# Optimization experiments

Hardware: AMD Instinct MI355X
Metric: run time of the kernel (lower is better)

The kernel has to match this reference:

```python
import jax, jax.numpy as jnp
import numpy as np

B, S, D, A = 8, 4096, 128, 128


def _pos_encoding(seq_len, dim):
    # sin/cos positional encoding, same construction as the torch buffer
    pos = np.arange(seq_len, dtype=np.float32)[:, None]
    div = np.exp(np.arange(0, dim, 2, dtype=np.float32) * (-np.log(10000.0) / dim))
    pe = np.zeros((seq_len, dim), dtype=np.float32)
    pe[:, 0::2] = np.sin(pos * div)
    pe[:, 1::2] = np.cos(pos * div)
    return jnp.asarray(pe)


def setup_inputs() -> dict:
    key = jax.random.key(0)
    ks = jax.random.split(key, 7)
    sc = 1.0 / np.sqrt(D)
    return {
        "x": jax.random.normal(ks[0], (B, S, D), dtype=jnp.float32),
        "Wq": jax.random.normal(ks[1], (D, A), dtype=jnp.float32) * sc,
        "bq": jnp.zeros((A,), dtype=jnp.float32),
        "Wk": jax.random.normal(ks[2], (D, A), dtype=jnp.float32) * sc,
        "bk": jnp.zeros((A,), dtype=jnp.float32),
        "Wv": jax.random.normal(ks[3], (D, A), dtype=jnp.float32) * sc,
        "bv": jnp.zeros((A,), dtype=jnp.float32),
    }


def reference(x, Wq, bq, Wk, bk, Wv, bv):
    b, s, d = x.shape
    pe = _pos_encoding(s, d)  # [S, D]
    xp = x + pe[None]  # broadcast add of positional encoding
    q = xp @ Wq + bq  # [B, S, A]
    k = xp @ Wk + bk
    v = xp @ Wv + bv
    scale = 1.0 / jnp.sqrt(jnp.asarray(Wq.shape[1], dtype=jnp.float32))
    scores = jnp.einsum("bsa,bta->bst", q, k) * scale  # [B, S, S]
    weights = jax.nn.softmax(scores, axis=-1)
    out = jnp.einsum("bst,bta->bsa", weights, v)  # [B, S, A]
    return out
```

## Files before the change

### kernel.cpp

```cpp
#include <hip/hip_runtime.h>

#define BB 8
#define SS 4096
#define DD 128

typedef __attribute__((ext_vector_type(8))) short v8s;
typedef __attribute__((ext_vector_type(4))) short v4s;
typedef __attribute__((ext_vector_type(4))) float v4f;
typedef __attribute__((ext_vector_type(16))) float v16f;

__device__ __forceinline__ unsigned short f2bf(float f) {
    unsigned int u = __float_as_uint(f);
    u += 0x7fffu + ((u >> 16) & 1u);
    return (unsigned short)(u >> 16);
}
__device__ __forceinline__ float bf2f(unsigned short s) {
    return __uint_as_float(((unsigned int)s) << 16);
}
__device__ __forceinline__ unsigned int pk_bf16(float a, float b) {
    unsigned int ua = __float_as_uint(a) + 0x8000u;
    unsigned int ub = __float_as_uint(b) + 0x8000u;
    return __builtin_amdgcn_perm(ub, ua, 0x07060302u);
}

#if !defined(__HIP_DEVICE_COMPILE__)
#define MFMA16(a, b, c) (c)
#define MFMA32(a, b, c) (c)
#else
#define MFMA16(a, b, c) __builtin_amdgcn_mfma_f32_16x16x32_bf16((a), (b), (c), 0, 0, 0)
#define MFMA32(a, b, c) __builtin_amdgcn_mfma_f32_32x32x16_bf16((a), (b), (c), 0, 0, 0)
#endif

#if !defined(__HIP_DEVICE_COMPILE__)
#define EXP2F(x) exp2f(x)
#elif __has_builtin(__builtin_amdgcn_exp2f)
#define EXP2F(x) __builtin_amdgcn_exp2f(x)
#else
#define EXP2F(x) exp2f(x)
#endif

#define QSCALE 0.12751743f
#define FIXM 24.0f

__global__ __launch_bounds__(256) void prep_w_kernel(
    const float* __restrict__ Wq, const float* __restrict__ Wk,
    const float* __restrict__ Wv, unsigned short* __restrict__ Wt)
{
    int id = blockIdx.x * 256 + threadIdx.x;
    int w = id >> 14;
    int n = (id >> 7) & 127;
    int k = id & 127;
    const float* W = (w == 0) ? Wq : (w == 1) ? Wk : Wv;
    Wt[id] = f2bf(W[k * 128 + n]);
}

__global__ __launch_bounds__(256, 3) void proj_kernel(
    const float* __restrict__ x, const unsigned short* __restrict__ Wt,
    const float* __restrict__ bq, const float* __restrict__ bk,
    const float* __restrict__ bv,
    unsigned short* __restrict__ qo, unsigned short* __restrict__ ko,
    unsigned short* __restrict__ vo)
{
    __shared__ __attribute__((aligned(16))) unsigned short o_q[64 * 136];
    __shared__ __attribute__((aligned(16))) unsigned short o_k[64 * 136];
    __shared__ __attribute__((aligned(16))) unsigned short o_v[128 * 72];

    const int tid = threadIdx.x;
    const int wave = tid >> 6;
    const int lane = tid & 63;
    const int quad = lane >> 4;
    const int l15 = lane & 15;
    const int rbase = blockIdx.x * 64;

    const int flatrow = rbase + wave * 16 + l15;
    const int srow = flatrow & 4095;
    v8s af[4];
#pragma unroll
    for (int kc = 0; kc < 4; ++kc) {
        const int kbase = kc * 32 + quad * 8;
        const v4f* xp = (const v4f*)(x + (size_t)flatrow * DD + kbase);
        v4f x0 = xp[0], x1 = xp[1];
        float xv[8] = {x0[0], x0[1], x0[2], x0[3], x1[0], x1[1], x1[2], x1[3]};
        v8s a;
#pragma unroll
        for (int j = 0; j < 8; ++j) {
            int d = kbase + j;
            float freq = __expf((float)(d & ~1) * -0.07195578415606394f);
            float arg = (float)srow * freq;
            float pe = (d & 1) ? __cosf(arg) : __sinf(arg);
            a[j] = (short)f2bf(xv[j] + pe);
        }
        af[kc] = a;
    }

#pragma unroll
    for (int mat = 0; mat < 3; ++mat) {
        const unsigned short* Wp = Wt + (mat << 14);
        const float* bias = (mat == 0) ? bq : (mat == 1) ? bk : bv;
#pragma unroll
        for (int nb = 0; nb < 8; ++nb) {
            const int col = nb * 16 + l15;
            v4f acc = {0.f, 0.f, 0.f, 0.f};
#pragma unroll
            for (int kc = 0; kc < 4; ++kc) {
                v8s bf = *(const v8s*)(Wp + col * 128 + kc * 32 + quad * 8);
                acc = MFMA16(af[kc], bf, acc);
            }
            float bval = bias[col];
#pragma unroll
            for (int reg = 0; reg < 4; ++reg) {
                int lr = wave * 16 + quad * 4 + reg;
                float val = acc[reg] + bval;
                if (mat == 0) {
                    o_q[lr * 136 + col] = f2bf(val * QSCALE);
                } else if (mat == 1) {
                    o_k[lr * 136 + col] = f2bf(val);
                } else {
                    o_v[col * 72 + lr] = f2bf(val);
                }
            }
        }
    }
    __syncthreads();

#pragma unroll
    for (int it = 0; it < 4; ++it) {
        int id = it * 256 + tid;
        int r = id >> 4, c8 = id & 15;
        *(v8s*)(qo + (size_t)(rbase + r) * DD + c8 * 8) =
            *(const v8s*)(o_q + r * 136 + c8 * 8);
        *(v8s*)(ko + (size_t)(rbase + r) * DD + c8 * 8) =
            *(const v8s*)(o_k + r * 136 + c8 * 8);
    }
    const int b0 = rbase >> 12, s0 = rbase & 4095;
#pragma unroll
    for (int it = 0; it < 4; ++it) {
        int id = it * 256 + tid;
        int a = id >> 3, c = id & 7;
        *(v8s*)(vo + ((size_t)(b0 * 128 + a)) * SS + s0 + c * 8) =
            *(const v8s*)(o_v + a * 72 + c * 8);
    }
}

#define KT 32
#define HKEYS 2048
#define NT (HKEYS / KT)
__global__ __launch_bounds__(256, 2) void flash_kernel(
    const unsigned short* __restrict__ qg,
    const unsigned short* __restrict__ kg,
    const unsigned short* __restrict__ vg,
    float* __restrict__ out,
    unsigned short* __restrict__ o2,
    float* __restrict__ statl)
{
    __shared__ __attribute__((aligned(16))) unsigned short k_lds[2][KT * 128];
    __shared__ __attribute__((aligned(16))) unsigned short v_lds[2][128 * KT];

    const int tid = threadIdx.x;
    const int wave = tid >> 6;
    const int lane = tid & 63;
    const int hi = lane >> 5;
    const int l31 = lane & 31;
    const int bid = blockIdx.x;
    const int b = bid & 7;
    const int half = (bid >> 3) & 1;
    const int qt = bid >> 4;
    const int qbase = qt * 128 + wave * 32;

    const size_t qrow = (size_t)(b * SS + qbase + l31) * DD;
    v8s qf[8];
#pragma unroll
    for (int kc = 0; kc < 8; ++kc)
        qf[kc] = *(const v8s*)(qg + qrow + kc * 16 + hi * 8);

    v16f o[4];
#pragma unroll
    for (int fg = 0; fg < 4; ++fg)
#pragma unroll
        for (int r = 0; r < 16; ++r) o[fg][r] = 0.f;
    float lrow = 0.f;

    const unsigned short* kb = kg + (size_t)b * SS * DD + (size_t)half * HKEYS * DD;
    const unsigned short* vb = vg + (size_t)b * DD * SS + half * HKEYS;

    const int kr_r = tid >> 4, kr_c = tid & 15;
    const int va = tid >> 2, vc8 = tid & 3;
    v8s kr[2], vr[2];

    auto load_tile = [&](int t) {
        const unsigned short* kp = kb + (size_t)t * KT * DD;
        const unsigned short* vp = vb + t * KT;
#pragma unroll
        for (int it = 0; it < 2; ++it) {
            kr[it] = *(const v8s*)(kp + (size_t)(kr_r + it * 16) * DD + kr_c * 8);
            vr[it] = *(const v8s*)(vp + (size_t)(va + it * 64) * SS + vc8 * 8);
        }
    };
    auto store_tile = [&](int p) {
#pragma unroll
        for (int it = 0; it < 2; ++it) {
            int r = kr_r + it * 16;
            *(v8s*)(&k_lds[p][r * 128 + ((kr_c ^ (r & 7)) << 3)]) = kr[it];
            int a = va + it * 64;
            v4s lo = {vr[it][0], vr[it][1], vr[it][2], vr[it][3]};
            v4s hv = {vr[it][4], vr[it][5], vr[it][6], vr[it][7]};
            int cc = vc8 >> 1, h = vc8 & 1;
            *(v4s*)(&v_lds[p][a * 32 + (((cc ^ (a & 3)) << 3) + h * 4)]) = lo;
            *(v4s*)(&v_lds[p][a * 32 + ((((cc + 2) ^ (a & 3)) << 3) + h * 4)]) = hv;
        }
    };
    auto compute = [&](int p) {
        v16f s;
#pragma unroll
        for (int r = 0; r < 16; ++r) s[r] = -FIXM;
#pragma unroll
        for (int kc = 0; kc < 8; ++kc) {
            v8s af = *(const v8s*)(&k_lds[p][l31 * 128 +
                                   (((kc * 2 + hi) ^ (l31 & 7)) << 3)]);
            s = MFMA32(af, qf[kc], s);
        }
        float e[16];
#pragma unroll
        for (int r = 0; r < 16; ++r) {
            e[r] = EXP2F(s[r]);
            lrow += e[r];
        }
        union { v8s v[2]; unsigned int u[8]; } P;
#pragma unroll
        for (int g = 0; g < 2; ++g)
#pragma unroll
            for (int m = 0; m < 4; ++m)
                P.u[g * 4 + m] = pk_bf16(e[2 * m + 8 * g], e[2 * m + 8 * g + 1]);
#pragma unroll
        for (int fg = 0; fg < 4; ++fg) {
            int row = fg * 32 + l31;
#pragma unroll
            for (int g = 0; g < 2; ++g) {
                v8s bf = *(const v8s*)(&v_lds[p][row * 32 +
                                       (((2 * hi + g) ^ (row & 3)) << 3)]);
                o[fg] = MFMA32(P.v[g], bf, o[fg]);
            }
        }
    };

    load_tile(0);
    store_tile(0);
    load_tile(1);
    __syncthreads();
#pragma unroll 1
    for (int kt = 0; kt < NT; kt += 2) {
        store_tile(1);
        if (kt + 2 < NT) load_tile(kt + 2);
        compute(0);
        __syncthreads();
        if (kt + 2 < NT) {
            store_tile(0);
            if (kt + 3 < NT) load_tile(kt + 3);
        }
        compute(1);
        __syncthreads();
    }

    lrow += __shfl_xor(lrow, 32, 64);
    if (lane < 32)
        statl[half * (BB * SS) + b * SS + qbase + l31] = lrow;
#pragma unroll
    for (int fg = 0; fg < 4; ++fg)
#pragma unroll
        for (int r = 0; r < 16; ++r) {
            int qr = (r & 3) + 8 * (r >> 2) + 4 * hi;
            size_t idx = (size_t)(b * SS + qbase + qr) * DD + fg * 32 + l31;
            if (half == 0) out[idx] = o[fg][r];
            else           o2[idx] = f2bf(o[fg][r]);
        }
}

__global__ __launch_bounds__(256) void combine_kernel(
    float* __restrict__ out, const unsigned short* __restrict__ o2,
    const float* __restrict__ statl)
{
    int id = blockIdx.x * 256 + threadIdx.x;
    int row = id >> 5;
    int c = (id & 31) * 4;
    float l1 = statl[row], l2 = statl[BB * SS + row];
    float inv = 1.0f / (l1 + l2);
    size_t base = (size_t)row * DD + c;
    v4f o1 = *(v4f*)(out + base);
    v4s p2 = *(const v4s*)(o2 + base);
    v4f r;
#pragma unroll
    for (int j = 0; j < 4; ++j)
        r[j] = (o1[j] + bf2f((unsigned short)p2[j])) * inv;
    *(v4f*)(out + base) = r;
}

extern "C" void kernel_launch(void* const* d_in, const int* in_sizes, int n_in,
                              void* d_out, int out_size, void* d_ws, size_t ws_size,
                              hipStream_t stream)
{
    const float* x  = (const float*)d_in[0];
    const float* Wq = (const float*)d_in[1];
    const float* bq = (const float*)d_in[2];
    const float* Wk = (const float*)d_in[3];
    const float* bk = (const float*)d_in[4];
    const float* Wv = (const float*)d_in[5];
    const float* bv = (const float*)d_in[6];
    float* out = (float*)d_out;

    unsigned short* Wt = (unsigned short*)d_ws;
    unsigned short* q  = Wt + 49152;
    unsigned short* k  = q + (size_t)BB * SS * DD;
    unsigned short* vT = k + (size_t)BB * SS * DD;
    unsigned short* O2 = vT + (size_t)BB * SS * DD;
    float* statl = (float*)(O2 + (size_t)BB * SS * DD);

    hipLaunchKernelGGL(prep_w_kernel, dim3(192), dim3(256), 0, stream, Wq, Wk, Wv, Wt);
    hipLaunchKernelGGL(proj_kernel, dim3(BB * SS / 64), dim3(256), 0, stream,
                       x, Wt, bq, bk, bv, q, k, vT);
    hipLaunchKernelGGL(flash_kernel, dim3(SS / 128 * 2 * BB), dim3(256), 0, stream,
                       q, k, vT, out, O2, statl);
    hipLaunchKernelGGL(combine_kernel, dim3(BB * SS * DD / 4 / 256), dim3(256), 0, stream,
                       out, O2, statl);
}
```

Before: 187.9 us.

## Split projection per matrix, precompute positional encoding, and reswizzle V LDS

A new kernel precomputes the positional-encoding table once into workspace. The projection kernel is then split so each block handles a single one of Q/K/V, with its weight matrix staged in LDS, giving three times as many blocks that each use less work and registers. This replaces the per-element sin/cos/exp work and the strided global weight reads. The cost is that x and pe are now re-read three times. The V tile swizzle in the flash kernel also gains an extra XOR term to reduce LDS bank conflicts.

Result: faster. 181.1 us (-3.6%).

```diff
diff --git a/kernel.cpp b/kernel.cpp
--- a/kernel.cpp
+++ b/kernel.cpp
@@ -54,23 +54,49 @@
     Wt[id] = f2bf(W[k * 128 + n]);
 }
 
+__global__ __launch_bounds__(256) void prep_pe_kernel(float* __restrict__ pe)
+{
+    int id = blockIdx.x * 256 + threadIdx.x;
+    int s = id >> 5;
+    int d0 = (id & 31) * 4;
+    v4f r;
+#pragma unroll
+    for (int j = 0; j < 4; j += 2) {
+        float freq = __expf((float)(d0 + j) * -0.07195578415606394f);
+        float arg = (float)s * freq;
+        r[j] = __sinf(arg);
+        r[j + 1] = __cosf(arg);
+    }
+    *(v4f*)(pe + (size_t)s * DD + d0) = r;
+}
+
 __global__ __launch_bounds__(256, 3) void proj_kernel(
-    const float* __restrict__ x, const unsigned short* __restrict__ Wt,
+    const float* __restrict__ x, const float* __restrict__ pe,
+    const unsigned short* __restrict__ Wt,
     const float* __restrict__ bq, const float* __restrict__ bk,
     const float* __restrict__ bv,
     unsigned short* __restrict__ qo, unsigned short* __restrict__ ko,
     unsigned short* __restrict__ vo)
 {
-    __shared__ __attribute__((aligned(16))) unsigned short o_q[64 * 136];
-    __shared__ __attribute__((aligned(16))) unsigned short o_k[64 * 136];
-    __shared__ __attribute__((aligned(16))) unsigned short o_v[128 * 72];
+    __shared__ __attribute__((aligned(16))) unsigned short w_lds[128 * 136];
+    __shared__ __attribute__((aligned(16))) unsigned short o_lds[9216];
 
     const int tid = threadIdx.x;
     const int wave = tid >> 6;
     const int lane = tid & 63;
     const int quad = lane >> 4;
     const int l15 = lane & 15;
-    const int rbase = blockIdx.x * 64;
+    const int bid = blockIdx.x;
+    const int mat = bid % 3;
+    const int rbase = (bid / 3) * 64;
+
+    const unsigned short* Wp = Wt + (mat << 14);
+#pragma unroll
+    for (int it = 0; it < 8; ++it) {
+        int id = it * 256 + tid;
+        int n = id >> 4, c8 = id & 15;
+        *(v8s*)(w_lds + n * 136 + c8 * 8) = *(const v8s*)(Wp + n * 128 + c8 * 8);
+    }
 
     const int flatrow = rbase + wave * 16 + l15;
     const int srow = flatrow & 4095;
@@ -79,66 +105,62 @@
     for (int kc = 0; kc < 4; ++kc) {
         const int kbase = kc * 32 + quad * 8;
         const v4f* xp = (const v4f*)(x + (size_t)flatrow * DD + kbase);
-        v4f x0 = xp[0], x1 = xp[1];
-        float xv[8] = {x0[0], x0[1], x0[2], x0[3], x1[0], x1[1], x1[2], x1[3]};
+        const v4f* pp = (const v4f*)(pe + (size_t)srow * DD + kbase);
+        v4f x0 = xp[0], x1 = xp[1], p0 = pp[0], p1 = pp[1];
         v8s a;
 #pragma unroll
-        for (int j = 0; j < 8; ++j) {
-            int d = kbase + j;
-            float freq = __expf((float)(d & ~1) * -0.07195578415606394f);
-            float arg = (float)srow * freq;
-            float pe = (d & 1) ? __cosf(arg) : __sinf(arg);
-            a[j] = (short)f2bf(xv[j] + pe);
-        }
+        for (int j = 0; j < 4; ++j) a[j] = (short)f2bf(x0[j] + p0[j]);
+#pragma unroll
+        for (int j = 0; j < 4; ++j) a[4 + j] = (short)f2bf(x1[j] + p1[j]);
         af[kc] = a;
     }
 
-#pragma unroll
-    for (int mat = 0; mat < 3; ++mat) {
-        const unsigned short* Wp = Wt + (mat << 14);
-        const float* bias = (mat == 0) ? bq : (mat == 1) ? bk : bv;
-#pragma unroll
-        for (int nb = 0; nb < 8; ++nb) {
-            const int col = nb * 16 + l15;
-            v4f acc = {0.f, 0.f, 0.f, 0.f};
-#pragma unroll
-            for (int kc = 0; kc < 4; ++kc) {
-                v8s bf = *(const v8s*)(Wp + col * 128 + kc * 32 + quad * 8);
-                acc = MFMA16(af[kc], bf, acc);
+    const float* bias = (mat == 0) ? bq : (mat == 1) ? bk : bv;
+    __syncthreads();
+
+#pragma unroll
+    for (int nb = 0; nb < 8; ++nb) {
+        const int col = nb * 16 + l15;
+        v4f acc = {0.f, 0.f, 0.f, 0.f};
+#pragma unroll
+        for (int kc = 0; kc < 4; ++kc) {
+            v8s bf = *(const v8s*)(w_lds + col * 136 + kc * 32 + quad * 8);
+            acc = MFMA16(af[kc], bf, acc);
+        }
+        float bval = bias[col];
+#pragma unroll
+        for (int reg = 0; reg < 4; ++reg) {
+            int lr = wave * 16 + quad * 4 + reg;
+            float val = acc[reg] + bval;
+            if (mat == 0) {
+                o_lds[lr * 136 + col] = f2bf(val * QSCALE);
+            } else if (mat == 1) {
+                o_lds[lr * 136 + col] = f2bf(val);
+            } else {
+                o_lds[col * 72 + lr] = f2bf(val);
             }
-            float bval = bias[col];
-#pragma unroll
-            for (int reg = 0; reg < 4; ++reg) {
-                int lr = wave * 16 + quad * 4 + reg;
-                float val = acc[reg] + bval;
-                if (mat == 0) {
-                    o_q[lr * 136 + col] = f2bf(val * QSCALE);
-                } else if (mat == 1) {
-                    o_k[lr * 136 + col] = f2bf(val);
-                } else {
-                    o_v[col * 72 + lr] = f2bf(val);
-                }
-            }
         }
     }
     __syncthreads();
 
-#pragma unroll
-    for (int it = 0; it < 4; ++it) {
-        int id = it * 256 + tid;
-        int r = id >> 4, c8 = id & 15;
-        *(v8s*)(qo + (size_t)(rbase + r) * DD + c8 * 8) =
-            *(const v8s*)(o_q + r * 136 + c8 * 8);
-        *(v8s*)(ko + (size_t)(rbase + r) * DD + c8 * 8) =
-            *(const v8s*)(o_k + r * 136 + c8 * 8);
-    }
-    const int b0 = rbase >> 12, s0 = rbase & 4095;
-#pragma unroll
-    for (int it = 0; it < 4; ++it) {
-        int id = it * 256 + tid;
-        int a = id >> 3, c = id & 7;
-        *(v8s*)(vo + ((size_t)(b0 * 128 + a)) * SS + s0 + c * 8) =
-            *(const v8s*)(o_v + a * 72 + c * 8);
+    if (mat <= 1) {
+        unsigned short* outp = (mat == 0) ? qo : ko;
+#pragma unroll
+        for (int it = 0; it < 4; ++it) {
+            int id = it * 256 + tid;
+            int r = id >> 4, c8 = id & 15;
+            *(v8s*)(outp + (size_t)(rbase + r) * DD + c8 * 8) =
+                *(const v8s*)(o_lds + r * 136 + c8 * 8);
+        }
+    } else {
+        const int b0 = rbase >> 12, s0 = rbase & 4095;
+#pragma unroll
+        for (int it = 0; it < 4; ++it) {
+            int id = it * 256 + tid;
+            int a = id >> 3, c = id & 7;
+            *(v8s*)(vo + ((size_t)(b0 * 128 + a)) * SS + s0 + c * 8) =
+                *(const v8s*)(o_lds + a * 72 + c * 8);
+        }
     }
 }
 
@@ -205,8 +227,9 @@
             v4s lo = {vr[it][0], vr[it][1], vr[it][2], vr[it][3]};
             v4s hv = {vr[it][4], vr[it][5], vr[it][6], vr[it][7]};
             int cc = vc8 >> 1, h = vc8 & 1;
-            *(v4s*)(&v_lds[p][a * 32 + (((cc ^ (a & 3)) << 3) + h * 4)]) = lo;
-            *(v4s*)(&v_lds[p][a * 32 + ((((cc + 2) ^ (a & 3)) << 3) + h * 4)]) = hv;
+            int sw = (a & 3) ^ ((a >> 2) & 1);
+            *(v4s*)(&v_lds[p][a * 32 + (((cc ^ sw) << 3) + h * 4)]) = lo;
+            *(v4s*)(&v_lds[p][a * 32 + ((((cc + 2) ^ sw) << 3) + h * 4)]) = hv;
         }
     };
     auto compute = [&](int p) {
@@ -234,10 +257,11 @@
 #pragma unroll
         for (int fg = 0; fg < 4; ++fg) {
             int row = fg * 32 + l31;
+            int sw = (row & 3) ^ ((row >> 2) & 1);
 #pragma unroll
             for (int g = 0; g < 2; ++g) {
                 v8s bf = *(const v8s*)(&v_lds[p][row * 32 +
-                                       (((2 * hi + g) ^ (row & 3)) << 3)]);
+                                       (((2 * hi + g) ^ sw) << 3)]);
                 o[fg] = MFMA32(P.v[g], bf, o[fg]);
             }
         }
@@ -313,10 +337,12 @@
     unsigned short* vT = k + (size_t)BB * SS * DD;
     unsigned short* O2 = vT + (size_t)BB * SS * DD;
     float* statl = (float*)(O2 + (size_t)BB * SS * DD);
+    float* pe    = statl + 2 * BB * SS;
 
     hipLaunchKernelGGL(prep_w_kernel, dim3(192), dim3(256), 0, stream, Wq, Wk, Wv, Wt);
-    hipLaunchKernelGGL(proj_kernel, dim3(BB * SS / 64), dim3(256), 0, stream,
-                       x, Wt, bq, bk, bv, q, k, vT);
+    hipLaunchKernelGGL(prep_pe_kernel, dim3(512), dim3(256), 0, stream, pe);
+    hipLaunchKernelGGL(proj_kernel, dim3(BB * SS / 64 * 3), dim3(256), 0, stream,
+                       x, pe, Wt, bq, bk, bv, q, k, vT);
     hipLaunchKernelGGL(flash_kernel, dim3(SS / 128 * 2 * BB), dim3(256), 0, stream,
                        q, k, vT, out, O2, statl);
     hipLaunchKernelGGL(combine_kernel, dim3(BB * SS * DD / 4 / 256), dim3(256), 0, stream,
```
